# Optimization experiments

Hardware: AMD Instinct MI355X
Metric: run time of the kernel (lower is better)

Reference implementation:

```python
import jax, jax.numpy as jnp
import numpy as np

HEADS = 4
OUT = 64  # hidden_channels


def gat_conv(x, src, dst, N, W, att_src, att_dst, bias):
    # x: [N, Fin] -> h: [N, H, C]
    h = (x @ W).reshape(N, HEADS, OUT)
    a_s = (h * att_src).sum(-1)  # [N, H]
    a_d = (h * att_dst).sum(-1)  # [N, H]
    logits = jax.nn.leaky_relu(a_s[src] + a_d[dst], negative_slope=0.2)  # [E, H]
    # segment softmax over incoming edges of each destination node
    m = jax.ops.segment_max(logits, dst, num_segments=N)
    e = jnp.exp(logits - m[dst])
    z = jax.ops.segment_sum(e, dst, num_segments=N)
    alpha = e / (z[dst] + 1e-16)
    out = jax.ops.segment_sum(h[src] * alpha[:, :, None], dst, num_segments=N)
    return out.reshape(N, HEADS * OUT) + bias


def setup_inputs() -> dict:
    key = jax.random.key(0)
    ks = jax.random.split(key, 16)
    N, E, F = 50000, 800000, 128
    HC = HEADS * OUT  # 256
    s = 0.1
    return {
        "x": jax.random.normal(ks[0], (N, F), jnp.float32),
        "edge_index": jax.random.randint(ks[1], (2, E), 0, N, dtype=jnp.int32),
        "W1": jax.random.normal(ks[2], (F, HC), jnp.float32) * s,
        "as1": jax.random.normal(ks[3], (1, HEADS, OUT), jnp.float32) * s,
        "ad1": jax.random.normal(ks[4], (1, HEADS, OUT), jnp.float32) * s,
        "b1": jnp.zeros((HC,), jnp.float32),
        "W2": jax.random.normal(ks[5], (HC, HC), jnp.float32) * s,
        "as2": jax.random.normal(ks[6], (1, HEADS, OUT), jnp.float32) * s,
        "ad2": jax.random.normal(ks[7], (1, HEADS, OUT), jnp.float32) * s,
        "b2": jnp.zeros((HC,), jnp.float32),
        "lw1": jax.random.normal(ks[8], (HC, OUT), jnp.float32) * s,
        "lb1": jnp.zeros((OUT,), jnp.float32),
        "lw2": jax.random.normal(ks[9], (OUT, 2), jnp.float32) * s,
        "lb2": jnp.zeros((2,), jnp.float32),
    }


def reference(x, edge_index, W1, as1, ad1, b1, W2, as2, ad2, b2, lw1, lb1, lw2, lb2):
    N = x.shape[0]
    # PyG GATConv default add_self_loops=True
    loop = jnp.arange(N, dtype=edge_index.dtype)
    src = jnp.concatenate([edge_index[0], loop])
    dst = jnp.concatenate([edge_index[1], loop])
    h = jax.nn.elu(gat_conv(x, src, dst, N, W1, as1, ad1, b1))
    # dropout is identity at inference
    h = jax.nn.elu(gat_conv(h, src, dst, N, W2, as2, ad2, b2))
    h = jax.nn.relu(h @ lw1 + lb1)
    return jax.nn.log_softmax(h @ lw2 + lb2, axis=1)
```

## Files before the change

### kernel.cpp

```cpp
#include <hip/hip_runtime.h>
#include <math.h>


typedef __attribute__((ext_vector_type(8))) _Float16 half8v;
typedef __attribute__((ext_vector_type(4))) float f32x4;

__device__ __forceinline__ float lrelu(float x) { return x > 0.f ? x : 0.2f * x; }
__device__ __forceinline__ float elu1(float x) { return x > 0.f ? x : (__expf(x) - 1.f); }

__global__ void convert_weights_kernel(const float* __restrict__ W1, const float* __restrict__ W2,
                                       const float* __restrict__ lw1,
                                       _Float16* __restrict__ o1, _Float16* __restrict__ o2,
                                       _Float16* __restrict__ o3) {
  int t = blockIdx.x * blockDim.x + threadIdx.x;
  if (t < 32768) {
    int n = t >> 7, k = t & 127;
    o1[t] = (_Float16)W1[(long)k * 256 + n];
  } else if (t < 98304) {
    int i = t - 32768;
    int n = i >> 8, k = i & 255;
    o2[i] = (_Float16)W2[(long)k * 256 + n];
  } else if (t < 114688) {
    int i = t - 98304;
    int n = i >> 8, k = i & 255;
    o3[i] = (_Float16)lw1[(long)k * 64 + n];
  }
}

__global__ void zero_int_kernel(int* __restrict__ p, int n) {
  int i = blockIdx.x * blockDim.x + threadIdx.x;
  if (i < n) p[i] = 0;
}

__global__ void count_kernel(const int* __restrict__ dst, int E, int* __restrict__ indeg) {
  int e = blockIdx.x * blockDim.x + threadIdx.x;
  if (e < E) atomicAdd(&indeg[dst[e]], 1);
}

__global__ void scan_block_kernel(const int* __restrict__ in, int* __restrict__ incl,
                                  int* __restrict__ bsum, int N) {
  __shared__ int wsum[16];
  int gid = blockIdx.x * 1024 + threadIdx.x;
  int lane = threadIdx.x & 63, w = threadIdx.x >> 6;
  int v = (gid < N) ? in[gid] : 0;
  int sv = v;
#pragma unroll
  for (int o = 1; o < 64; o <<= 1) {
    int t = __shfl_up(sv, o);
    if (lane >= o) sv += t;
  }
  if (lane == 63) wsum[w] = sv;
  __syncthreads();
  if (w == 0) {
    int bs = (lane < 16) ? wsum[lane] : 0;
#pragma unroll
    for (int o = 1; o < 16; o <<= 1) {
      int t = __shfl_up(bs, o);
      if (lane >= o) bs += t;
    }
    if (lane < 16) wsum[lane] = bs;
  }
  __syncthreads();
  if (w > 0) sv += wsum[w - 1];
  if (gid < N) incl[gid] = sv;
  if (threadIdx.x == 1023) bsum[blockIdx.x] = sv;
}

__global__ void scan_finalize_kernel(const int* __restrict__ in, const int* __restrict__ incl,
                                     const int* __restrict__ bsum, int* __restrict__ off,
                                     int* __restrict__ cursor, int N) {
  int gid = blockIdx.x * blockDim.x + threadIdx.x;
  if (gid >= N) return;
  int b = gid >> 10;
  int carry = 0;
  for (int k = 0; k < b; ++k) carry += bsum[k];
  int ic = incl[gid] + carry;
  off[gid + 1] = ic;
  cursor[gid] = ic - in[gid];
  if (gid == 0) off[0] = 0;
}

__global__ void fill_kernel(const int* __restrict__ src, const int* __restrict__ dst, int E,
                            int* __restrict__ cursor, int* __restrict__ csr_src) {
  int e = blockIdx.x * blockDim.x + threadIdx.x;
  if (e < E) {
    int pos = atomicAdd(&cursor[dst[e]], 1);
    csr_src[pos] = src[e];
  }
}

template <typename AT>
__launch_bounds__(256)
__global__ void mfma_gemm_attn_kernel(const AT* __restrict__ A,
                                      const _Float16* __restrict__ B,
                                      const float* __restrict__ att_s,
                                      const float* __restrict__ att_d,
                                      _Float16* __restrict__ C,
                                      float* __restrict__ a_s, float* __restrict__ a_d,
                                      int M, int K) {
  __shared__ _Float16 As[64][40];
  __shared__ _Float16 Bs[64][40];
  int tid = threadIdx.x;
  int bm = blockIdx.y * 64, bn = blockIdx.x * 64;
  int lane = tid & 63, wave = tid >> 6;
  int srow = tid >> 2, sch = (tid & 3) * 8;
  const AT* Ap = A + (long)(bm + srow) * K + sch;
  const _Float16* Bp = B + (long)(bn + srow) * K + sch;
  bool arow_ok = (bm + srow) < M;
  int fm = lane & 15, fq = lane >> 4;
  f32x4 acc[4];
#pragma unroll
  for (int cb = 0; cb < 4; ++cb) acc[cb] = (f32x4){0.f, 0.f, 0.f, 0.f};
  for (int k0 = 0; k0 < K; k0 += 32) {
    half8v a8 = {0, 0, 0, 0, 0, 0, 0, 0};
    if (arow_ok) {
      if constexpr (sizeof(AT) == 4) {
        float4 f0 = *(const float4*)(Ap + k0);
        float4 f1 = *(const float4*)(Ap + k0 + 4);
        a8 = (half8v){(_Float16)f0.x, (_Float16)f0.y, (_Float16)f0.z, (_Float16)f0.w,
                      (_Float16)f1.x, (_Float16)f1.y, (_Float16)f1.z, (_Float16)f1.w};
      } else {
        a8 = *(const half8v*)(Ap + k0);
      }
    }
    uint4 vb = *(const uint4*)(Bp + k0);
    *(half8v*)&As[srow][sch] = a8;
    *(uint4*)&Bs[srow][sch] = vb;
    __syncthreads();
    half8v ah = *(const half8v*)&As[wave * 16 + fm][fq * 8];
#pragma unroll
    for (int cb = 0; cb < 4; ++cb) {
      half8v bh = *(const half8v*)&Bs[cb * 16 + fm][fq * 8];
      acc[cb] = __builtin_amdgcn_mfma_f32_16x16x32_f16(ah, bh, acc[cb], 0, 0, 0);
    }
    __syncthreads();
  }
  int row0 = bm + wave * 16 + fq * 4;
  int headi = bn >> 6;
  float asv[4], adv[4];
#pragma unroll
  for (int cb = 0; cb < 4; ++cb) {
    int col = bn + cb * 16 + fm;
    asv[cb] = att_s[col];
    adv[cb] = att_d[col];
  }
#pragma unroll
  for (int r = 0; r < 4; ++r) {
    int row = row0 + r;
    float sp = 0.f, dp = 0.f;
#pragma unroll
    for (int cb = 0; cb < 4; ++cb) {
      float v = acc[cb][r];
      sp = fmaf(v, asv[cb], sp);
      dp = fmaf(v, adv[cb], dp);
      if (row < M) C[(long)row * 256 + bn + cb * 16 + fm] = (_Float16)v;
    }
#pragma unroll
    for (int o = 1; o < 16; o <<= 1) {
      sp += __shfl_xor(sp, o);
      dp += __shfl_xor(dp, o);
    }
    if (fm == 0 && row < M) {
      a_s[(long)row * 4 + headi] = sp;
      a_d[(long)row * 4 + headi] = dp;
    }
  }
}

__launch_bounds__(256)
__global__ void head_mfma_kernel(const _Float16* __restrict__ A, const _Float16* __restrict__ B,
                                 const float* __restrict__ lb1, const float* __restrict__ lw2,
                                 const float* __restrict__ lb2, float* __restrict__ out, int M) {
  __shared__ _Float16 As[64][40];
  __shared__ _Float16 Bs[64][40];
  int tid = threadIdx.x;
  int bm = blockIdx.x * 64;
  int lane = tid & 63, wave = tid >> 6;
  int srow = tid >> 2, sch = (tid & 3) * 8;
  const _Float16* Ap = A + (long)(bm + srow) * 256 + sch;
  const _Float16* Bp = B + (long)srow * 256 + sch;
  int fm = lane & 15, fq = lane >> 4;
  f32x4 acc[4];
#pragma unroll
  for (int cb = 0; cb < 4; ++cb) acc[cb] = (f32x4){0.f, 0.f, 0.f, 0.f};
  for (int k0 = 0; k0 < 256; k0 += 32) {
    uint4 va = *(const uint4*)(Ap + k0);
    uint4 vb = *(const uint4*)(Bp + k0);
    *(uint4*)&As[srow][sch] = va;
    *(uint4*)&Bs[srow][sch] = vb;
    __syncthreads();
    half8v ah = *(const half8v*)&As[wave * 16 + fm][fq * 8];
#pragma unroll
    for (int cb = 0; cb < 4; ++cb) {
      half8v bh = *(const half8v*)&Bs[cb * 16 + fm][fq * 8];
      acc[cb] = __builtin_amdgcn_mfma_f32_16x16x32_f16(ah, bh, acc[cb], 0, 0, 0);
    }
    __syncthreads();
  }
  float lb1c[4], w20[4], w21[4];
#pragma unroll
  for (int cb = 0; cb < 4; ++cb) {
    int col = cb * 16 + fm;
    lb1c[cb] = lb1[col];
    w20[cb] = lw2[col * 2 + 0];
    w21[cb] = lw2[col * 2 + 1];
  }
  float b20 = lb2[0], b21 = lb2[1];
#pragma unroll
  for (int r = 0; r < 4; ++r) {
    float v0 = 0.f, v1 = 0.f;
#pragma unroll
    for (int cb = 0; cb < 4; ++cb) {
      float s = fmaxf(acc[cb][r] + lb1c[cb], 0.f);
      v0 = fmaf(s, w20[cb], v0);
      v1 = fmaf(s, w21[cb], v1);
    }
#pragma unroll
    for (int o = 1; o < 16; o <<= 1) {
      v0 += __shfl_xor(v0, o);
      v1 += __shfl_xor(v1, o);
    }
    if (fm == 0) {
      int row = bm + wave * 16 + fq * 4 + r;
      if (row < M) {
        v0 += b20;
        v1 += b21;
        float mx = fmaxf(v0, v1);
        float ls = mx + logf(expf(v0 - mx) + expf(v1 - mx));
        out[(long)row * 2 + 0] = v0 - ls;
        out[(long)row * 2 + 1] = v1 - ls;
      }
    }
  }
}

__launch_bounds__(256)
__global__ void gat_aggregate5_kernel(const _Float16* __restrict__ h,
                                      const float* __restrict__ a_s,
                                      const float* __restrict__ a_d,
                                      const int* __restrict__ off,
                                      const int* __restrict__ csr_src,
                                      const float* __restrict__ bias,
                                      _Float16* __restrict__ outp, int N) {
  int wid = (blockIdx.x * blockDim.x + threadIdx.x) >> 6;
  int lane = threadIdx.x & 63;
  if (wid >= N) return;
  int c = lane & 31, hlf = lane >> 5, head4 = c >> 3;
  int h1 = lane & 3, sl1 = lane >> 2;
  int beg = off[wid], cnt = off[wid + 1] - beg;
  float ad_h1 = a_d[wid * 4 + h1];
  float self_l = lrelu(a_s[wid * 4 + h1] + ad_h1);
  float m = self_l;
  for (int c0 = sl1; c0 < cnt; c0 += 16) {
    int s = csr_src[beg + c0];
    m = fmaxf(m, lrelu(a_s[(long)s * 4 + h1] + ad_h1));
  }
  m = fmaxf(m, __shfl_xor(m, 4));
  m = fmaxf(m, __shfl_xor(m, 8));
  m = fmaxf(m, __shfl_xor(m, 16));
  m = fmaxf(m, __shfl_xor(m, 32));
  float mh = __shfl(m, head4);
  float selfc = __shfl(self_l, head4);
  float acc[8] = {};
  float z = 0.f;
  if (hlf == 0) {
    z = __expf(selfc - mh);
    half8v sr = *(const half8v*)(h + (long)wid * 256 + c * 8);
#pragma unroll
    for (int i = 0; i < 8; ++i) acc[i] = z * (float)sr[i];
  }
  for (int c0 = 0; c0 < cnt; c0 += 16) {
    int i2 = c0 + (lane & 15);
    int sv = (i2 < cnt) ? csr_src[beg + i2] : 0;
    int i1 = c0 + sl1;
    int sp = __shfl(sv, sl1);
    float pv = 0.f;
    if (i1 < cnt) pv = __expf(lrelu(a_s[(long)sp * 4 + h1] + ad_h1) - m);
#pragma unroll
    for (int j = 0; j < 16; j += 2) {
      if (c0 + j >= cnt) break;
      int e = j + hlf;
      int s = __shfl(sv, e);
      float p = __shfl(pv, e * 4 + head4);
      z += p;
      half8v rv = *(const half8v*)(h + (long)s * 256 + c * 8);
      acc[0] = fmaf(p, (float)rv[0], acc[0]);
      acc[1] = fmaf(p, (float)rv[1], acc[1]);
      acc[2] = fmaf(p, (float)rv[2], acc[2]);
      acc[3] = fmaf(p, (float)rv[3], acc[3]);
      acc[4] = fmaf(p, (float)rv[4], acc[4]);
      acc[5] = fmaf(p, (float)rv[5], acc[5]);
      acc[6] = fmaf(p, (float)rv[6], acc[6]);
      acc[7] = fmaf(p, (float)rv[7], acc[7]);
    }
  }
  z += __shfl_xor(z, 32);
#pragma unroll
  for (int i = 0; i < 8; ++i) acc[i] += __shfl_xor(acc[i], 32);
  if (hlf == 0) {
    float inv = 1.f / z;
    half8v o;
#pragma unroll
    for (int i = 0; i < 8; ++i) o[i] = (_Float16)elu1(fmaf(acc[i], inv, bias[c * 8 + i]));
    *(half8v*)(outp + (long)wid * 256 + c * 8) = o;
  }
}

static inline int cdiv(int a, int b) { return (a + b - 1) / b; }

extern "C" void kernel_launch(void* const* d_in, const int* in_sizes, int n_in,
                              void* d_out, int out_size, void* d_ws, size_t ws_size,
                              hipStream_t stream) {
  const float* x = (const float*)d_in[0];
  const int* ei = (const int*)d_in[1];
  const float* W1 = (const float*)d_in[2];
  const float* as1 = (const float*)d_in[3];
  const float* ad1 = (const float*)d_in[4];
  const float* b1 = (const float*)d_in[5];
  const float* W2 = (const float*)d_in[6];
  const float* as2 = (const float*)d_in[7];
  const float* ad2 = (const float*)d_in[8];
  const float* b2 = (const float*)d_in[9];
  const float* lw1 = (const float*)d_in[10];
  const float* lb1 = (const float*)d_in[11];
  const float* lw2 = (const float*)d_in[12];
  const float* lb2 = (const float*)d_in[13];
  float* out = (float*)d_out;

  int N = in_sizes[0] / 128;
  int E = in_sizes[1] / 2;
  int Mp = cdiv(N, 64) * 64;

  char* ws = (char*)d_ws;
  _Float16* Wt1 = (_Float16*)ws; ws += 256 * 128 * 2;
  _Float16* Wt2 = (_Float16*)ws; ws += 256 * 256 * 2;
  _Float16* WL = (_Float16*)ws; ws += 64 * 256 * 2;
  _Float16* C = (_Float16*)ws; ws += (size_t)Mp * 256 * 2;
  _Float16* h2 = (_Float16*)ws; ws += (size_t)Mp * 256 * 2;
  float* aS = (float*)ws; ws += (size_t)N * 4 * 4;
  float* aD = (float*)ws; ws += (size_t)N * 4 * 4;
  int* csr_src = (int*)ws; ws += (size_t)E * 4;
  int* indeg = (int*)ws; ws += (size_t)N * 4;
  int* cursor = (int*)ws; ws += (size_t)N * 4;
  int* off = (int*)ws; ws += (size_t)(N + 4) * 4;
  int* incl = (int*)ws; ws += (size_t)N * 4;
  int* bsum = (int*)ws; ws += 64 * 4;

  const int* e_src = ei;
  const int* e_dst = ei + E;
  int nb = cdiv(N, 1024);

  convert_weights_kernel<<<cdiv(114688, 256), 256, 0, stream>>>(W1, W2, lw1, Wt1, Wt2, WL);

  zero_int_kernel<<<cdiv(N, 256), 256, 0, stream>>>(indeg, N);
  count_kernel<<<cdiv(E, 256), 256, 0, stream>>>(e_dst, E, indeg);
  scan_block_kernel<<<nb, 1024, 0, stream>>>(indeg, incl, bsum, N);
  scan_finalize_kernel<<<cdiv(N, 256), 256, 0, stream>>>(indeg, incl, bsum, off, cursor, N);
  fill_kernel<<<cdiv(E, 256), 256, 0, stream>>>(e_src, e_dst, E, cursor, csr_src);

  mfma_gemm_attn_kernel<float><<<dim3(4, Mp / 64), 256, 0, stream>>>(x, Wt1, as1, ad1, C, aS, aD,
                                                                     N, 128);
  gat_aggregate5_kernel<<<cdiv(N, 4), 256, 0, stream>>>(C, aS, aD, off, csr_src, b1, h2, N);

  mfma_gemm_attn_kernel<_Float16><<<dim3(4, Mp / 64), 256, 0, stream>>>(h2, Wt2, as2, ad2, C, aS,
                                                                        aD, N, 256);
  gat_aggregate5_kernel<<<cdiv(N, 4), 256, 0, stream>>>(C, aS, aD, off, csr_src, b2, h2, N);

  head_mfma_kernel<<<Mp / 64, 256, 0, stream>>>(h2, WL, lb1, lw2, lb2, out, N);
}
```

Measured before the change: 377.4 us.

## Fuse GAT aggregation into the following GEMM and the MLP head

Each block now aggregates 64 destination nodes into a shared-memory tile and immediately multiplies that tile by the next layer's weights. The GEMM epilogue also computes the attention dot products, and the last aggregation feeds the head MLP and log-softmax directly. This removes the global write and re-read of each layer's aggregated features and cuts two kernel launches. In exchange, far fewer waves run at once, with each wave processing 16 nodes one after another, so the latency-bound neighbour gather gets less parallelism to hide memory latency. Load imbalance across blocks may also increase.

```diff
diff --git a/kernel.cpp b/kernel.cpp
--- a/kernel.cpp
+++ b/kernel.cpp
@@ -89,9 +89,8 @@
   }
 }
 
-template <typename AT>
 __launch_bounds__(256)
-__global__ void mfma_gemm_attn_kernel(const AT* __restrict__ A,
+__global__ void mfma_gemm_attn_kernel(const float* __restrict__ A,
                                       const _Float16* __restrict__ B,
                                       const float* __restrict__ att_s,
                                       const float* __restrict__ att_d,
@@ -104,7 +103,7 @@
   int bm = blockIdx.y * 64, bn = blockIdx.x * 64;
   int lane = tid & 63, wave = tid >> 6;
   int srow = tid >> 2, sch = (tid & 3) * 8;
-  const AT* Ap = A + (long)(bm + srow) * K + sch;
+  const float* Ap = A + (long)(bm + srow) * K + sch;
   const _Float16* Bp = B + (long)(bn + srow) * K + sch;
   bool arow_ok = (bm + srow) < M;
   int fm = lane & 15, fq = lane >> 4;
@@ -114,14 +113,10 @@
   for (int k0 = 0; k0 < K; k0 += 32) {
     half8v a8 = {0, 0, 0, 0, 0, 0, 0, 0};
     if (arow_ok) {
-      if constexpr (sizeof(AT) == 4) {
-        float4 f0 = *(const float4*)(Ap + k0);
-        float4 f1 = *(const float4*)(Ap + k0 + 4);
-        a8 = (half8v){(_Float16)f0.x, (_Float16)f0.y, (_Float16)f0.z, (_Float16)f0.w,
-                      (_Float16)f1.x, (_Float16)f1.y, (_Float16)f1.z, (_Float16)f1.w};
-      } else {
-        a8 = *(const half8v*)(Ap + k0);
-      }
+      float4 f0 = *(const float4*)(Ap + k0);
+      float4 f1 = *(const float4*)(Ap + k0 + 4);
+      a8 = (half8v){(_Float16)f0.x, (_Float16)f0.y, (_Float16)f0.z, (_Float16)f0.w,
+                    (_Float16)f1.x, (_Float16)f1.y, (_Float16)f1.z, (_Float16)f1.w};
     }
     uint4 vb = *(const uint4*)(Bp + k0);
     *(half8v*)&As[srow][sch] = a8;
@@ -167,84 +162,13 @@
   }
 }
 
-__launch_bounds__(256)
-__global__ void head_mfma_kernel(const _Float16* __restrict__ A, const _Float16* __restrict__ B,
-                                 const float* __restrict__ lb1, const float* __restrict__ lw2,
-                                 const float* __restrict__ lb2, float* __restrict__ out, int M) {
-  __shared__ _Float16 As[64][40];
-  __shared__ _Float16 Bs[64][40];
-  int tid = threadIdx.x;
-  int bm = blockIdx.x * 64;
-  int lane = tid & 63, wave = tid >> 6;
-  int srow = tid >> 2, sch = (tid & 3) * 8;
-  const _Float16* Ap = A + (long)(bm + srow) * 256 + sch;
-  const _Float16* Bp = B + (long)srow * 256 + sch;
-  int fm = lane & 15, fq = lane >> 4;
-  f32x4 acc[4];
-#pragma unroll
-  for (int cb = 0; cb < 4; ++cb) acc[cb] = (f32x4){0.f, 0.f, 0.f, 0.f};
-  for (int k0 = 0; k0 < 256; k0 += 32) {
-    uint4 va = *(const uint4*)(Ap + k0);
-    uint4 vb = *(const uint4*)(Bp + k0);
-    *(uint4*)&As[srow][sch] = va;
-    *(uint4*)&Bs[srow][sch] = vb;
-    __syncthreads();
-    half8v ah = *(const half8v*)&As[wave * 16 + fm][fq * 8];
-#pragma unroll
-    for (int cb = 0; cb < 4; ++cb) {
-      half8v bh = *(const half8v*)&Bs[cb * 16 + fm][fq * 8];
-      acc[cb] = __builtin_amdgcn_mfma_f32_16x16x32_f16(ah, bh, acc[cb], 0, 0, 0);
-    }
-    __syncthreads();
-  }
-  float lb1c[4], w20[4], w21[4];
-#pragma unroll
-  for (int cb = 0; cb < 4; ++cb) {
-    int col = cb * 16 + fm;
-    lb1c[cb] = lb1[col];
-    w20[cb] = lw2[col * 2 + 0];
-    w21[cb] = lw2[col * 2 + 1];
-  }
-  float b20 = lb2[0], b21 = lb2[1];
-#pragma unroll
-  for (int r = 0; r < 4; ++r) {
-    float v0 = 0.f, v1 = 0.f;
-#pragma unroll
-    for (int cb = 0; cb < 4; ++cb) {
-      float s = fmaxf(acc[cb][r] + lb1c[cb], 0.f);
-      v0 = fmaf(s, w20[cb], v0);
-      v1 = fmaf(s, w21[cb], v1);
-    }
-#pragma unroll
-    for (int o = 1; o < 16; o <<= 1) {
-      v0 += __shfl_xor(v0, o);
-      v1 += __shfl_xor(v1, o);
-    }
-    if (fm == 0) {
-      int row = bm + wave * 16 + fq * 4 + r;
-      if (row < M) {
-        v0 += b20;
-        v1 += b21;
-        float mx = fmaxf(v0, v1);
-        float ls = mx + logf(expf(v0 - mx) + expf(v1 - mx));
-        out[(long)row * 2 + 0] = v0 - ls;
-        out[(long)row * 2 + 1] = v1 - ls;
-      }
-    }
-  }
-}
-
-__launch_bounds__(256)
-__global__ void gat_aggregate5_kernel(const _Float16* __restrict__ h,
-                                      const float* __restrict__ a_s,
-                                      const float* __restrict__ a_d,
-                                      const int* __restrict__ off,
-                                      const int* __restrict__ csr_src,
-                                      const float* __restrict__ bias,
-                                      _Float16* __restrict__ outp, int N) {
-  int wid = (blockIdx.x * blockDim.x + threadIdx.x) >> 6;
-  int lane = threadIdx.x & 63;
-  if (wid >= N) return;
+__device__ __forceinline__ void aggregate_node(const _Float16* __restrict__ h,
+                                               const float* __restrict__ a_s,
+                                               const float* __restrict__ a_d,
+                                               const int* __restrict__ off,
+                                               const int* __restrict__ csr_src,
+                                               const float* __restrict__ bias,
+                                               int wid, int lane, float out8[8]) {
   int c = lane & 31, hlf = lane >> 5, head4 = c >> 3;
   int h1 = lane & 3, sl1 = lane >> 2;
   int beg = off[wid], cnt = off[wid + 1] - beg;
@@ -297,12 +221,176 @@
   z += __shfl_xor(z, 32);
 #pragma unroll
   for (int i = 0; i < 8; ++i) acc[i] += __shfl_xor(acc[i], 32);
-  if (hlf == 0) {
-    float inv = 1.f / z;
-    half8v o;
-#pragma unroll
-    for (int i = 0; i < 8; ++i) o[i] = (_Float16)elu1(fmaf(acc[i], inv, bias[c * 8 + i]));
-    *(half8v*)(outp + (long)wid * 256 + c * 8) = o;
+  float inv = 1.f / z;
+#pragma unroll
+  for (int i = 0; i < 8; ++i) out8[i] = elu1(fmaf(acc[i], inv, bias[c * 8 + i]));
+}
+
+__launch_bounds__(256)
+__global__ void agg_gemm_attn_kernel(const _Float16* __restrict__ h,
+                                     const float* __restrict__ a_s_in,
+                                     const float* __restrict__ a_d_in,
+                                     const int* __restrict__ off,
+                                     const int* __restrict__ csr_src,
+                                     const float* __restrict__ bias,
+                                     const _Float16* __restrict__ B,
+                                     const float* __restrict__ att_s,
+                                     const float* __restrict__ att_d,
+                                     _Float16* __restrict__ C,
+                                     float* __restrict__ a_s_out,
+                                     float* __restrict__ a_d_out, int N) {
+  __shared__ _Float16 As[64][264];
+  __shared__ _Float16 Bs[64][40];
+  int tid = threadIdx.x;
+  int lane = tid & 63, wave = tid >> 6;
+  int bm = blockIdx.x * 64;
+  int c = lane & 31, hlf = lane >> 5;
+#pragma unroll 1
+  for (int i = 0; i < 16; ++i) {
+    int row = wave * 16 + i;
+    int node = bm + row;
+    float o8[8] = {};
+    if (node < N) aggregate_node(h, a_s_in, a_d_in, off, csr_src, bias, node, lane, o8);
+    if (hlf == 0) {
+      half8v v;
+#pragma unroll
+      for (int k = 0; k < 8; ++k) v[k] = (_Float16)o8[k];
+      *(half8v*)&As[row][c * 8] = v;
+    }
+  }
+  int fm = lane & 15, fq = lane >> 4;
+  int srow = tid >> 2, sch = (tid & 3) * 8;
+#pragma unroll 1
+  for (int bn4 = 0; bn4 < 4; ++bn4) {
+    int bn = bn4 * 64;
+    f32x4 acc[4];
+#pragma unroll
+    for (int cb = 0; cb < 4; ++cb) acc[cb] = (f32x4){0.f, 0.f, 0.f, 0.f};
+    for (int k0 = 0; k0 < 256; k0 += 32) {
+      uint4 vb = *(const uint4*)(B + (long)(bn + srow) * 256 + k0 + sch);
+      __syncthreads();
+      *(uint4*)&Bs[srow][sch] = vb;
+      __syncthreads();
+      half8v ah = *(const half8v*)&As[wave * 16 + fm][k0 + fq * 8];
+#pragma unroll
+      for (int cb = 0; cb < 4; ++cb) {
+        half8v bh = *(const half8v*)&Bs[cb * 16 + fm][fq * 8];
+        acc[cb] = __builtin_amdgcn_mfma_f32_16x16x32_f16(ah, bh, acc[cb], 0, 0, 0);
+      }
+    }
+    int row0 = bm + wave * 16 + fq * 4;
+    float asv[4], adv[4];
+#pragma unroll
+    for (int cb = 0; cb < 4; ++cb) {
+      int col = bn + cb * 16 + fm;
+      asv[cb] = att_s[col];
+      adv[cb] = att_d[col];
+    }
+#pragma unroll
+    for (int r = 0; r < 4; ++r) {
+      int row = row0 + r;
+      float sp = 0.f, dp = 0.f;
+#pragma unroll
+      for (int cb = 0; cb < 4; ++cb) {
+        float v = acc[cb][r];
+        sp = fmaf(v, asv[cb], sp);
+        dp = fmaf(v, adv[cb], dp);
+        if (row < N) C[(long)row * 256 + bn + cb * 16 + fm] = (_Float16)v;
+      }
+#pragma unroll
+      for (int o = 1; o < 16; o <<= 1) {
+        sp += __shfl_xor(sp, o);
+        dp += __shfl_xor(dp, o);
+      }
+      if (fm == 0 && row < N) {
+        a_s_out[(long)row * 4 + bn4] = sp;
+        a_d_out[(long)row * 4 + bn4] = dp;
+      }
+    }
+  }
+}
+
+__launch_bounds__(256)
+__global__ void agg_head_kernel(const _Float16* __restrict__ h,
+                                const float* __restrict__ a_s_in,
+                                const float* __restrict__ a_d_in,
+                                const int* __restrict__ off,
+                                const int* __restrict__ csr_src,
+                                const float* __restrict__ bias,
+                                const _Float16* __restrict__ B,
+                                const float* __restrict__ lb1, const float* __restrict__ lw2,
+                                const float* __restrict__ lb2, float* __restrict__ out, int N) {
+  __shared__ _Float16 As[64][264];
+  __shared__ _Float16 Bs[64][40];
+  int tid = threadIdx.x;
+  int lane = tid & 63, wave = tid >> 6;
+  int bm = blockIdx.x * 64;
+  int c = lane & 31, hlf = lane >> 5;
+#pragma unroll 1
+  for (int i = 0; i < 16; ++i) {
+    int row = wave * 16 + i;
+    int node = bm + row;
+    float o8[8] = {};
+    if (node < N) aggregate_node(h, a_s_in, a_d_in, off, csr_src, bias, node, lane, o8);
+    if (hlf == 0) {
+      half8v v;
+#pragma unroll
+      for (int k = 0; k < 8; ++k) v[k] = (_Float16)o8[k];
+      *(half8v*)&As[row][c * 8] = v;
+    }
+  }
+  __syncthreads();
+  int fm = lane & 15, fq = lane >> 4;
+  int srow = tid >> 2, sch = (tid & 3) * 8;
+  f32x4 acc[4];
+#pragma unroll
+  for (int cb = 0; cb < 4; ++cb) acc[cb] = (f32x4){0.f, 0.f, 0.f, 0.f};
+  for (int k0 = 0; k0 < 256; k0 += 32) {
+    uint4 vb = *(const uint4*)(B + (long)srow * 256 + k0 + sch);
+    if (k0) __syncthreads();
+    *(uint4*)&Bs[srow][sch] = vb;
+    __syncthreads();
+    half8v ah = *(const half8v*)&As[wave * 16 + fm][k0 + fq * 8];
+#pragma unroll
+    for (int cb = 0; cb < 4; ++cb) {
+      half8v bh = *(const half8v*)&Bs[cb * 16 + fm][fq * 8];
+      acc[cb] = __builtin_amdgcn_mfma_f32_16x16x32_f16(ah, bh, acc[cb], 0, 0, 0);
+    }
+  }
+  float lb1c[4], w20[4], w21[4];
+#pragma unroll
+  for (int cb = 0; cb < 4; ++cb) {
+    int col = cb * 16 + fm;
+    lb1c[cb] = lb1[col];
+    w20[cb] = lw2[col * 2 + 0];
+    w21[cb] = lw2[col * 2 + 1];
+  }
+  float b20 = lb2[0], b21 = lb2[1];
+#pragma unroll
+  for (int r = 0; r < 4; ++r) {
+    float v0 = 0.f, v1 = 0.f;
+#pragma unroll
+    for (int cb = 0; cb < 4; ++cb) {
+      float s = fmaxf(acc[cb][r] + lb1c[cb], 0.f);
+      v0 = fmaf(s, w20[cb], v0);
+      v1 = fmaf(s, w21[cb], v1);
+    }
+#pragma unroll
+    for (int o = 1; o < 16; o <<= 1) {
+      v0 += __shfl_xor(v0, o);
+      v1 += __shfl_xor(v1, o);
+    }
+    if (fm == 0) {
+      int row = bm + wave * 16 + fq * 4 + r;
+      if (row < N) {
+        v0 += b20;
+        v1 += b21;
+        float mx = fmaxf(v0, v1);
+        float ls = mx + logf(expf(v0 - mx) + expf(v1 - mx));
+        out[(long)row * 2 + 0] = v0 - ls;
+        out[(long)row * 2 + 1] = v1 - ls;
+      }
+    }
   }
 }
 
@@ -335,10 +423,12 @@
   _Float16* Wt1 = (_Float16*)ws; ws += 256 * 128 * 2;
   _Float16* Wt2 = (_Float16*)ws; ws += 256 * 256 * 2;
   _Float16* WL = (_Float16*)ws; ws += 64 * 256 * 2;
-  _Float16* C = (_Float16*)ws; ws += (size_t)Mp * 256 * 2;
-  _Float16* h2 = (_Float16*)ws; ws += (size_t)Mp * 256 * 2;
-  float* aS = (float*)ws; ws += (size_t)N * 4 * 4;
-  float* aD = (float*)ws; ws += (size_t)N * 4 * 4;
+  _Float16* C1 = (_Float16*)ws; ws += (size_t)Mp * 256 * 2;
+  _Float16* C2 = (_Float16*)ws; ws += (size_t)Mp * 256 * 2;
+  float* aS1 = (float*)ws; ws += (size_t)N * 4 * 4;
+  float* aD1 = (float*)ws; ws += (size_t)N * 4 * 4;
+  float* aS2 = (float*)ws; ws += (size_t)N * 4 * 4;
+  float* aD2 = (float*)ws; ws += (size_t)N * 4 * 4;
   int* csr_src = (int*)ws; ws += (size_t)E * 4;
   int* indeg = (int*)ws; ws += (size_t)N * 4;
   int* cursor = (int*)ws; ws += (size_t)N * 4;
@@ -358,13 +448,10 @@
   scan_finalize_kernel<<<cdiv(N, 256), 256, 0, stream>>>(indeg, incl, bsum, off, cursor, N);
   fill_kernel<<<cdiv(E, 256), 256, 0, stream>>>(e_src, e_dst, E, cursor, csr_src);
 
-  mfma_gemm_attn_kernel<float><<<dim3(4, Mp / 64), 256, 0, stream>>>(x, Wt1, as1, ad1, C, aS, aD,
-                                                                     N, 128);
-  gat_aggregate5_kernel<<<cdiv(N, 4), 256, 0, stream>>>(C, aS, aD, off, csr_src, b1, h2, N);
-
-  mfma_gemm_attn_kernel<_Float16><<<dim3(4, Mp / 64), 256, 0, stream>>>(h2, Wt2, as2, ad2, C, aS,
-                                                                        aD, N, 256);
-  gat_aggregate5_kernel<<<cdiv(N, 4), 256, 0, stream>>>(C, aS, aD, off, csr_src, b2, h2, N);
-
-  head_mfma_kernel<<<Mp / 64, 256, 0, stream>>>(h2, WL, lb1, lw2, lb2, out, N);
-}
+  mfma_gemm_attn_kernel<<<dim3(4, Mp / 64), 256, 0, stream>>>(x, Wt1, as1, ad1, C1, aS1, aD1,
+                                                              N, 128);
+  agg_gemm_attn_kernel<<<Mp / 64, 256, 0, stream>>>(C1, aS1, aD1, off, csr_src, b1, Wt2, as2, ad2,
+                                                    C2, aS2, aD2, N);
+  agg_head_kernel<<<Mp / 64, 256, 0, stream>>>(C2, aS2, aD2, off, csr_src, b2, WL, lb1, lw2, lb2,
+                                               out, N);
+}
```

Result: slower. 462.3 us (+22.5%).
